# Kernel optimization log

Hardware: AMD Instinct MI355X
Metric: run time of the kernel (lower is better)

## Reference

```python
import jax, jax.numpy as jnp
import numpy as np

BS, T, F, D_IN, NH, D_OUT = 8, 32, 128, 64, 8, 64
GAUSS_STD = 2.0


def setup_inputs() -> dict:
    key = jax.random.key(0)
    ks = jax.random.split(key, 9)
    X = jax.random.normal(ks[0], (BS, F, T, D_IN), dtype=jnp.float32)
    W_query = jax.random.normal(ks[1], (T, F, D_IN, NH, 2), dtype=jnp.float32)
    W_key = jax.random.normal(ks[2], (T, F, D_IN, NH, 2), dtype=jnp.float32)
    Wkey_ = jax.random.normal(ks[3], (T, 2, 2), dtype=jnp.float32)
    u = jax.random.normal(ks[4], (T, F, 2), dtype=jnp.float32)
    attention_center = GAUSS_STD * jax.random.normal(ks[5], (T, NH, 1), dtype=jnp.float32)
    alpha = jax.random.normal(ks[6], (T,), dtype=jnp.float32)
    # relative position features: [F, F, 2] = (delta^2, delta), tiled over T
    rel = (jnp.arange(F)[None, :] - jnp.arange(F)[:, None]).astype(jnp.float32)
    R = jnp.broadcast_to(jnp.stack([rel ** 2, rel], axis=-1)[None], (T, F, F, 2))
    W = jax.random.normal(ks[7], (T, NH * D_IN, D_OUT), dtype=jnp.float32)
    b = jax.random.normal(ks[8], (F, T, D_OUT), dtype=jnp.float32)
    return {"X": X, "W_query": W_query, "W_key": W_key, "Wkey_": Wkey_,
            "u": u, "attention_center": attention_center, "alpha": alpha,
            "R": R, "W": W, "b": b}


def reference(X, W_query, W_key, Wkey_, u, attention_center, alpha, R, W, b):
    # X: [bs, F, T, d_in] -> [bs, T, F, d_in]
    Xp = jnp.transpose(X, (0, 2, 1, 3))
    bs = Xp.shape[0]
    query = jnp.einsum('btfd,tfdhe->btfhe', Xp, W_query)  # [bs,T,F,Nh,2]
    key_t = jnp.einsum('btfd,tfdhe->btfhe', Xp, W_key)    # [bs,T,F,Nh,2]
    r_delta = jnp.einsum('tde,tfle->tfld', Wkey_, R)      # [T,F,F,2]
    centers = jnp.concatenate([jnp.ones_like(attention_center),
                               -2.0 * attention_center], axis=-1)  # [T,Nh,2]
    v = -alpha[:, None, None] * centers                   # [T,Nh,2]
    scores = (jnp.einsum('btfhe,btlhe->btfhl', query, key_t)
              + jnp.einsum('btfhe,tfle->btfhl', query, r_delta)
              + jnp.einsum('tle,btfhe->btfhl', u, key_t)
              + jnp.einsum('the,tfle->tfhl', v, r_delta)[None])  # [bs,T,F,Nh,F]
    probs = jax.nn.softmax(scores, axis=-1)
    vals = jnp.einsum('btfhl,btld->btfhd', probs, Xp)     # [bs,T,F,Nh,d_in]
    vals = vals.reshape(bs, T, F, NH * D_IN)
    out = jnp.einsum('btfd,tdo->bfto', vals, W) + b[None]  # [bs,F,T,d_out]
    return out
```

## Files before the change

kernel.cpp:

```cpp
#include <hip/hip_runtime.h>
#include <hip/hip_bf16.h>

#define NBS 8
#define NT 32
#define NF 128
#define NDIN 64
#define NNH 8
#define NDOUT 64

typedef __bf16 bf16_t;
typedef __bf16 bf16x8 __attribute__((ext_vector_type(8)));
typedef float f32x4 __attribute__((ext_vector_type(4)));

__global__ __launch_bounds__(256, 4)
void qk_project_kernel(const float* __restrict__ X,
                       const float* __restrict__ Wq,
                       const float* __restrict__ Wk,
                       float* __restrict__ q_ws,
                       float* __restrict__ k_ws)
{
    __shared__ float lx[4][8][64];
    const int w = threadIdx.x >> 6, lane = threadIdx.x & 63;
    const int gw = blockIdx.x * 4 + w;
    const int t = gw >> 7, f = gw & 127;

    {
        const int b = lane >> 3, d8 = (lane & 7) << 3;
        const float* src = &X[(((size_t)b * NF + f) * NT + t) * NDIN + d8];
        const float4 v0 = *(const float4*)src;
        const float4 v1 = *(const float4*)(src + 4);
        *(float4*)&lx[w][b][d8]     = v0;
        *(float4*)&lx[w][b][d8 + 4] = v1;
    }
    __syncthreads();

    const int dq = lane >> 4, he = lane & 15;
    const float* wq = Wq + ((size_t)t * NF + f) * (NDIN * 16);
    const float* wk = Wk + ((size_t)t * NF + f) * (NDIN * 16);
    float qa[8] = {0,0,0,0,0,0,0,0}, ka[8] = {0,0,0,0,0,0,0,0};
    for (int d0 = 0; d0 < NDIN; d0 += 4) {
        const int d = d0 + dq;
        const float wqv = wq[d * 16 + he];
        const float wkv = wk[d * 16 + he];
#pragma unroll
        for (int b = 0; b < 8; ++b) {
            const float x = lx[w][b][d];
            qa[b] = fmaf(x, wqv, qa[b]);
            ka[b] = fmaf(x, wkv, ka[b]);
        }
    }
#pragma unroll
    for (int b = 0; b < 8; ++b) {
        qa[b] += __shfl_xor(qa[b], 16); qa[b] += __shfl_xor(qa[b], 32);
        ka[b] += __shfl_xor(ka[b], 16); ka[b] += __shfl_xor(ka[b], 32);
    }
#pragma unroll
    for (int bb = 0; bb < 2; ++bb) {
        const int b = dq + bb * 4;
        q_ws[(((size_t)b * NT + t) * 16 + he) * NF + f] = qa[b];
        k_ws[(((size_t)b * NT + t) * 16 + he) * NF + f] = ka[b];
    }
}

__global__ __launch_bounds__(512, 2)
void spatial_attn_kernel(const float* __restrict__ X,
                         const float* __restrict__ q_ws,
                         const float* __restrict__ k_ws,
                         const float* __restrict__ Wkey,
                         const float* __restrict__ U,
                         const float* __restrict__ AC,
                         const float* __restrict__ Alpha,
                         const float* __restrict__ Wo,
                         const float* __restrict__ Bias,
                         float* __restrict__ Out)
{
    const int blk  = blockIdx.x;
    const int b    = blk & 7;
    const int t    = blk >> 3;
    const int tid  = threadIdx.x;
    const int w    = tid >> 6;
    const int lane = tid & 63;
    const int cq   = lane & 15;
    const int rq   = lane >> 4;
    const int rt   = w;
    const int frow = 16 * rt + cq;

    __shared__ __align__(16) unsigned char smem[142336];
    bf16_t (*XT)[NF + 8]        = (bf16_t (*)[NF + 8])(smem);
    float4 (*kv)[136]           = (float4 (*)[136])(smem + 17408);
    float4 (*qf)[128]           = (float4 (*)[128])(smem + 34816);
    bf16_t (*WTall)[NDOUT][72]  = (bf16_t (*)[NDOUT][72])(smem + 51200);
    bf16_t (*Vscr)[16][68]      = (bf16_t (*)[16][68])(smem + 124928);

#pragma unroll
    for (int r = 0; r < 4; ++r) {
        const int idx = tid + r * 512;
        const int f = idx >> 4, d4 = (idx & 15) << 2;
        const float4 v = *(const float4*)&X[(((size_t)b * NF + f) * NT + t) * NDIN + d4];
        XT[d4 + 0][f] = (bf16_t)v.x; XT[d4 + 1][f] = (bf16_t)v.y;
        XT[d4 + 2][f] = (bf16_t)v.z; XT[d4 + 3][f] = (bf16_t)v.w;
    }
#pragma unroll
    for (int r = 0; r < 2; ++r) {
        const int idx = tid + r * 512;
        const int hh = idx >> 7, l = idx & 127;
        const size_t qkb = ((size_t)b * NT + t) * 16;
        const float k0 = k_ws[(qkb + 2 * hh + 0) * NF + l];
        const float k1 = k_ws[(qkb + 2 * hh + 1) * NF + l];
        const float2 u01 = *(const float2*)&U[((size_t)t * NF + l) * 2];
        kv[hh][17 * (l >> 4) + (l & 15)] = make_float4(k0, k1, u01.x, u01.y);
        const float q0 = q_ws[(qkb + 2 * hh + 0) * NF + l];
        const float q1 = q_ws[(qkb + 2 * hh + 1) * NF + l];
        qf[hh][l] = make_float4(q0, q1, k0, k1);
    }
#pragma unroll
    for (int rep = 0; rep < 16; ++rep) {
        const int flat = rep * 512 + tid;
        const int h = flat >> 10, f10 = flat & 1023;
        const int d = f10 >> 4, o4 = (f10 & 15) << 2;
        const float4 v = *(const float4*)&Wo[((size_t)t * 512 + h * 64 + d) * NDOUT + o4];
        WTall[h][o4 + 0][d] = (bf16_t)v.x; WTall[h][o4 + 1][d] = (bf16_t)v.y;
        WTall[h][o4 + 2][d] = (bf16_t)v.z; WTall[h][o4 + 3][d] = (bf16_t)v.w;
    }

    const float alpha_t = Alpha[t];
    const float wk00 = Wkey[t * 4 + 0], wk01 = Wkey[t * 4 + 1];
    const float wk10 = Wkey[t * 4 + 2], wk11 = Wkey[t * 4 + 3];

    __syncthreads();

    f32x4 oacc[4] = { {0.f,0.f,0.f,0.f}, {0.f,0.f,0.f,0.f}, {0.f,0.f,0.f,0.f}, {0.f,0.f,0.f,0.f} };

#pragma unroll 1
    for (int h = 0; h < NNH; ++h) {
        const float4 qq = qf[h][frow];
        const float q0 = qq.x, q1 = qq.y, kf0 = qq.z, kf1 = qq.w;
        const float v1 = 2.f * alpha_t * AC[t * NNH + h];
        const float c0 = (q0 - alpha_t) * wk00 + (q1 + v1) * wk10;
        const float c1 = (q0 - alpha_t) * wk01 + (q1 + v1) * wk11;

        float sc[4][8];
        float rowmax = -3.0e38f;
#pragma unroll
        for (int kt = 0; kt < 4; ++kt) {
            const int s  = kt * 2 + (rq >> 1);
            const int i0 = (rq & 1) << 3;
            const float4* kvp = &kv[h][17 * s + i0];
            float del = (float)(kt * 32 + rq * 8 - frow);
#pragma unroll
            for (int j = 0; j < 8; ++j) {
                const float4 kj = kvp[j];
                const float sv = q0 * kj.x + q1 * kj.y + kf0 * kj.z + kf1 * kj.w
                               + (c0 * del + c1) * del;
                sc[kt][j] = sv;
                rowmax = fmaxf(rowmax, sv);
                del += 1.f;
            }
        }
        rowmax = fmaxf(rowmax, __shfl_xor(rowmax, 16));
        rowmax = fmaxf(rowmax, __shfl_xor(rowmax, 32));
        float sum = 0.f;
#pragma unroll
        for (int kt = 0; kt < 4; ++kt)
#pragma unroll
            for (int j = 0; j < 8; ++j) {
                sc[kt][j] = __expf(sc[kt][j] - rowmax);
                sum += sc[kt][j];
            }
        sum += __shfl_xor(sum, 16);
        sum += __shfl_xor(sum, 32);
        const float rinv = 1.f / sum;

        f32x4 vacc[4] = { {0.f,0.f,0.f,0.f}, {0.f,0.f,0.f,0.f}, {0.f,0.f,0.f,0.f}, {0.f,0.f,0.f,0.f} };
#pragma unroll
        for (int kt = 0; kt < 4; ++kt) {
            bf16x8 pf;
#pragma unroll
            for (int j = 0; j < 8; ++j) pf[j] = (bf16_t)(sc[kt][j] * rinv);
#pragma unroll
            for (int ct = 0; ct < 4; ++ct) {
                const bf16x8 bb = *(const bf16x8*)&XT[ct * 16 + cq][kt * 32 + rq * 8];
                vacc[ct] = __builtin_amdgcn_mfma_f32_16x16x32_bf16(pf, bb, vacc[ct], 0, 0, 0);
            }
        }
#pragma unroll
        for (int ct = 0; ct < 4; ++ct)
#pragma unroll
            for (int rr = 0; rr < 4; ++rr)
                Vscr[w][rq * 4 + rr][ct * 16 + cq] = (bf16_t)vacc[ct][rr];

#pragma unroll
        for (int kt = 0; kt < 2; ++kt) {
            const bf16x8 a = *(const bf16x8*)&Vscr[w][cq][kt * 32 + rq * 8];
#pragma unroll
            for (int ct = 0; ct < 4; ++ct) {
                const bf16x8 bw = *(const bf16x8*)&WTall[h][ct * 16 + cq][kt * 32 + rq * 8];
                oacc[ct] = __builtin_amdgcn_mfma_f32_16x16x32_bf16(a, bw, oacc[ct], 0, 0, 0);
            }
        }
    }

#pragma unroll
    for (int ct = 0; ct < 4; ++ct) {
#pragma unroll
        for (int rr = 0; rr < 4; ++rr) {
            const int f = 16 * rt + rq * 4 + rr;
            const int o = ct * 16 + cq;
            Out[(((size_t)b * NF + f) * NT + t) * NDOUT + o] =
                oacc[ct][rr] + Bias[((size_t)f * NT + t) * NDOUT + o];
        }
    }
}

extern "C" void kernel_launch(void* const* d_in, const int* in_sizes, int n_in,
                              void* d_out, int out_size, void* d_ws, size_t ws_size,
                              hipStream_t stream) {
    (void)in_sizes; (void)n_in; (void)ws_size; (void)out_size;
    const float* X    = (const float*)d_in[0];
    const float* Wq   = (const float*)d_in[1];
    const float* Wk   = (const float*)d_in[2];
    const float* Wkey = (const float*)d_in[3];
    const float* U    = (const float*)d_in[4];
    const float* AC   = (const float*)d_in[5];
    const float* Al   = (const float*)d_in[6];
    const float* Wo   = (const float*)d_in[8];
    const float* Bias = (const float*)d_in[9];

    float* q_ws = (float*)d_ws;
    float* k_ws = q_ws + (size_t)NBS * NT * 16 * NF;

    qk_project_kernel<<<dim3(NT * NF / 4), dim3(256), 0, stream>>>(X, Wq, Wk, q_ws, k_ws);
    spatial_attn_kernel<<<dim3(NBS * NT), dim3(512), 0, stream>>>(
        X, q_ws, k_ws, Wkey, U, AC, Al, Wo, Bias, (float*)d_out);
}
```

Measured before the change: 54.40 us.

## Split heads across two blocks with atomic output reduction and double-buffered Wo

Each (batch, time) tile is now handled by two blocks that each process four heads, doubling the grid from 256 to 512 blocks. Partial outputs are combined with atomicAdd into an output zeroed by a memset, and only the first head group adds the bias. Wo is streamed per head into a double-buffered, XOR-swizzled shared tile instead of being staged in full, which cuts shared memory enough to allow higher occupancy. The X transpose is swizzled as well. The costs are an extra memset, atomic traffic, a barrier on every head iteration, and X being loaded twice per tile.

```diff
diff --git a/kernel.cpp b/kernel.cpp
--- a/kernel.cpp
+++ b/kernel.cpp
@@ -62,7 +62,7 @@
     }
 }
 
-__global__ __launch_bounds__(512, 2)
+__global__ __launch_bounds__(512, 4)
 void spatial_attn_kernel(const float* __restrict__ X,
                          const float* __restrict__ q_ws,
                          const float* __restrict__ k_ws,
@@ -76,7 +76,9 @@
 {
     const int blk  = blockIdx.x;
     const int b    = blk & 7;
-    const int t    = blk >> 3;
+    const int tq   = blk >> 3;
+    const int hg   = tq & 1;
+    const int t    = tq >> 1;
     const int tid  = threadIdx.x;
     const int w    = tid >> 6;
     const int lane = tid & 63;
@@ -85,42 +87,50 @@
     const int rt   = w;
     const int frow = 16 * rt + cq;
 
-    __shared__ __align__(16) unsigned char smem[142336];
-    bf16_t (*XT)[NF + 8]        = (bf16_t (*)[NF + 8])(smem);
-    float4 (*kv)[136]           = (float4 (*)[136])(smem + 17408);
-    float4 (*qf)[128]           = (float4 (*)[128])(smem + 34816);
-    bf16_t (*WTall)[NDOUT][72]  = (bf16_t (*)[NDOUT][72])(smem + 51200);
-    bf16_t (*Vscr)[16][68]      = (bf16_t (*)[16][68])(smem + 124928);
+    __shared__ __align__(16) unsigned char smem[62992];
+    bf16_t* XTs        = (bf16_t*)smem;
+    float4 (*kv)[136]  = (float4 (*)[136])(smem + 16384);
+    float2 (*qls)[128] = (float2 (*)[128])(smem + 25088);
+    float*  acs        = (float*)(smem + 29184);
+    bf16_t* WTs        = (bf16_t*)(smem + 29200);
+    bf16_t (*Vscr)[16][68] = (bf16_t (*)[16][68])(smem + 45584);
 
 #pragma unroll
     for (int r = 0; r < 4; ++r) {
         const int idx = tid + r * 512;
         const int f = idx >> 4, d4 = (idx & 15) << 2;
         const float4 v = *(const float4*)&X[(((size_t)b * NF + f) * NT + t) * NDIN + d4];
-        XT[d4 + 0][f] = (bf16_t)v.x; XT[d4 + 1][f] = (bf16_t)v.y;
-        XT[d4 + 2][f] = (bf16_t)v.z; XT[d4 + 3][f] = (bf16_t)v.w;
-    }
+        float vv[4]; vv[0] = v.x; vv[1] = v.y; vv[2] = v.z; vv[3] = v.w;
+#pragma unroll
+        for (int i = 0; i < 4; ++i) {
+            const int d = d4 + i;
+            XTs[d * 128 + (((f >> 3) ^ (d & 15)) << 3) + (f & 7)] = (bf16_t)vv[i];
+        }
+    }
+    {
+        const int hh = tid >> 7, l = tid & 127;
+        const int h = hg * 4 + hh;
+        const size_t qkb = ((size_t)b * NT + t) * 16;
+        const float k0 = k_ws[(qkb + 2 * h + 0) * NF + l];
+        const float k1 = k_ws[(qkb + 2 * h + 1) * NF + l];
+        const float2 u01 = *(const float2*)&U[((size_t)t * NF + l) * 2];
+        kv[hh][17 * (l >> 4) + (l & 15)] = make_float4(k0, k1, u01.x, u01.y);
+        const float q0 = q_ws[(qkb + 2 * h + 0) * NF + l];
+        const float q1 = q_ws[(qkb + 2 * h + 1) * NF + l];
+        qls[hh][l] = make_float2(q0, q1);
+    }
+    if (tid < 4) acs[tid] = AC[t * NNH + hg * 4 + tid];
 #pragma unroll
     for (int r = 0; r < 2; ++r) {
         const int idx = tid + r * 512;
-        const int hh = idx >> 7, l = idx & 127;
-        const size_t qkb = ((size_t)b * NT + t) * 16;
-        const float k0 = k_ws[(qkb + 2 * hh + 0) * NF + l];
-        const float k1 = k_ws[(qkb + 2 * hh + 1) * NF + l];
-        const float2 u01 = *(const float2*)&U[((size_t)t * NF + l) * 2];
-        kv[hh][17 * (l >> 4) + (l & 15)] = make_float4(k0, k1, u01.x, u01.y);
-        const float q0 = q_ws[(qkb + 2 * hh + 0) * NF + l];
-        const float q1 = q_ws[(qkb + 2 * hh + 1) * NF + l];
-        qf[hh][l] = make_float4(q0, q1, k0, k1);
-    }
-#pragma unroll
-    for (int rep = 0; rep < 16; ++rep) {
-        const int flat = rep * 512 + tid;
-        const int h = flat >> 10, f10 = flat & 1023;
-        const int d = f10 >> 4, o4 = (f10 & 15) << 2;
-        const float4 v = *(const float4*)&Wo[((size_t)t * 512 + h * 64 + d) * NDOUT + o4];
-        WTall[h][o4 + 0][d] = (bf16_t)v.x; WTall[h][o4 + 1][d] = (bf16_t)v.y;
-        WTall[h][o4 + 2][d] = (bf16_t)v.z; WTall[h][o4 + 3][d] = (bf16_t)v.w;
+        const int dd = idx >> 4, o4 = (idx & 15) << 2;
+        const float4 v = *(const float4*)&Wo[((size_t)t * 512 + (hg * 4) * 64 + dd) * NDOUT + o4];
+        float vv[4]; vv[0] = v.x; vv[1] = v.y; vv[2] = v.z; vv[3] = v.w;
+#pragma unroll
+        for (int i = 0; i < 4; ++i) {
+            const int o = o4 + i;
+            WTs[o * 64 + (((dd >> 3) ^ (o & 7)) << 3) + (dd & 7)] = (bf16_t)vv[i];
+        }
     }
 
     const float alpha_t = Alpha[t];
@@ -132,10 +142,28 @@
     f32x4 oacc[4] = { {0.f,0.f,0.f,0.f}, {0.f,0.f,0.f,0.f}, {0.f,0.f,0.f,0.f}, {0.f,0.f,0.f,0.f} };
 
 #pragma unroll 1
-    for (int h = 0; h < NNH; ++h) {
-        const float4 qq = qf[h][frow];
-        const float q0 = qq.x, q1 = qq.y, kf0 = qq.z, kf1 = qq.w;
-        const float v1 = 2.f * alpha_t * AC[t * NNH + h];
+    for (int th = 0; th < 4; ++th) {
+        if (th < 3) {
+            const int hn = hg * 4 + th + 1;
+            const int bn = ((th + 1) & 1) * 4096;
+#pragma unroll
+            for (int r = 0; r < 2; ++r) {
+                const int idx = tid + r * 512;
+                const int dd = idx >> 4, o4 = (idx & 15) << 2;
+                const float4 v = *(const float4*)&Wo[((size_t)t * 512 + hn * 64 + dd) * NDOUT + o4];
+                float vv[4]; vv[0] = v.x; vv[1] = v.y; vv[2] = v.z; vv[3] = v.w;
+#pragma unroll
+                for (int i = 0; i < 4; ++i) {
+                    const int o = o4 + i;
+                    WTs[bn + o * 64 + (((dd >> 3) ^ (o & 7)) << 3) + (dd & 7)] = (bf16_t)vv[i];
+                }
+            }
+        }
+        const int buf = (th & 1) * 4096;
+        const float2 qq = qls[th][frow];
+        const float4 kk = kv[th][17 * (frow >> 4) + (frow & 15)];
+        const float q0 = qq.x, q1 = qq.y, kf0 = kk.x, kf1 = kk.y;
+        const float v1 = 2.f * alpha_t * acs[th];
         const float c0 = (q0 - alpha_t) * wk00 + (q1 + v1) * wk10;
         const float c1 = (q0 - alpha_t) * wk01 + (q1 + v1) * wk11;
 
@@ -145,7 +173,7 @@
         for (int kt = 0; kt < 4; ++kt) {
             const int s  = kt * 2 + (rq >> 1);
             const int i0 = (rq & 1) << 3;
-            const float4* kvp = &kv[h][17 * s + i0];
+            const float4* kvp = &kv[th][17 * s + i0];
             float del = (float)(kt * 32 + rq * 8 - frow);
 #pragma unroll
             for (int j = 0; j < 8; ++j) {
@@ -179,7 +207,7 @@
             for (int j = 0; j < 8; ++j) pf[j] = (bf16_t)(sc[kt][j] * rinv);
 #pragma unroll
             for (int ct = 0; ct < 4; ++ct) {
-                const bf16x8 bb = *(const bf16x8*)&XT[ct * 16 + cq][kt * 32 + rq * 8];
+                const bf16x8 bb = *(const bf16x8*)&XTs[(ct * 16 + cq) * 128 + (((kt * 4 + rq) ^ cq) << 3)];
                 vacc[ct] = __builtin_amdgcn_mfma_f32_16x16x32_bf16(pf, bb, vacc[ct], 0, 0, 0);
             }
         }
@@ -194,10 +222,11 @@
             const bf16x8 a = *(const bf16x8*)&Vscr[w][cq][kt * 32 + rq * 8];
 #pragma unroll
             for (int ct = 0; ct < 4; ++ct) {
-                const bf16x8 bw = *(const bf16x8*)&WTall[h][ct * 16 + cq][kt * 32 + rq * 8];
+                const bf16x8 bw = *(const bf16x8*)&WTs[buf + (ct * 16 + cq) * 64 + (((kt * 4 + rq) ^ (cq & 7)) << 3)];
                 oacc[ct] = __builtin_amdgcn_mfma_f32_16x16x32_bf16(a, bw, oacc[ct], 0, 0, 0);
             }
         }
+        __syncthreads();
     }
 
 #pragma unroll
@@ -206,8 +235,9 @@
         for (int rr = 0; rr < 4; ++rr) {
             const int f = 16 * rt + rq * 4 + rr;
             const int o = ct * 16 + cq;
-            Out[(((size_t)b * NF + f) * NT + t) * NDOUT + o] =
-                oacc[ct][rr] + Bias[((size_t)f * NT + t) * NDOUT + o];
+            float val = oacc[ct][rr];
+            if (hg == 0) val += Bias[((size_t)f * NT + t) * NDOUT + o];
+            atomicAdd(&Out[(((size_t)b * NF + f) * NT + t) * NDOUT + o], val);
         }
     }
 }
@@ -215,7 +245,7 @@
 extern "C" void kernel_launch(void* const* d_in, const int* in_sizes, int n_in,
                               void* d_out, int out_size, void* d_ws, size_t ws_size,
                               hipStream_t stream) {
-    (void)in_sizes; (void)n_in; (void)ws_size; (void)out_size;
+    (void)in_sizes; (void)n_in; (void)ws_size;
     const float* X    = (const float*)d_in[0];
     const float* Wq   = (const float*)d_in[1];
     const float* Wk   = (const float*)d_in[2];
@@ -229,7 +259,8 @@
     float* q_ws = (float*)d_ws;
     float* k_ws = q_ws + (size_t)NBS * NT * 16 * NF;
 
+    hipMemsetAsync(d_out, 0, (size_t)out_size * sizeof(float), stream);
     qk_project_kernel<<<dim3(NT * NF / 4), dim3(256), 0, stream>>>(X, Wq, Wk, q_ws, k_ws);
-    spatial_attn_kernel<<<dim3(NBS * NT), dim3(512), 0, stream>>>(
+    spatial_attn_kernel<<<dim3(NBS * NT * 2), dim3(512), 0, stream>>>(
         X, q_ws, k_ws, Wkey, U, AC, Al, Wo, Bias, (float*)d_out);
 }
```

New measurement: 132.9 us. 2.44x slower.

## Swizzle shared-memory layouts for XT, WT and key buffers and pack score math

Applied to the files above, without the earlier changes.

Replaces padded shared arrays for the transposed X and W tiles with XOR-swizzled unpadded layouts, and repacks key/u values into pair-interleaved 12-float records so two adjacent score columns load with two float4 reads. Score computation is rewritten on float2 vectors so the compiler can use packed FP32 arithmetic. The aim is fewer LDS bank conflicts, fewer LDS instructions, and fewer scalar FP ops in the softmax stage, at the cost of more complex indexing.

```diff
diff --git a/kernel.cpp b/kernel.cpp
--- a/kernel.cpp
+++ b/kernel.cpp
@@ -11,6 +11,7 @@
 typedef __bf16 bf16_t;
 typedef __bf16 bf16x8 __attribute__((ext_vector_type(8)));
 typedef float f32x4 __attribute__((ext_vector_type(4)));
+typedef float f32x2 __attribute__((ext_vector_type(2)));
 
 __global__ __launch_bounds__(256, 4)
 void qk_project_kernel(const float* __restrict__ X,
@@ -85,20 +86,24 @@
     const int rt   = w;
     const int frow = 16 * rt + cq;
 
-    __shared__ __align__(16) unsigned char smem[142336];
-    bf16_t (*XT)[NF + 8]        = (bf16_t (*)[NF + 8])(smem);
-    float4 (*kv)[136]           = (float4 (*)[136])(smem + 17408);
-    float4 (*qf)[128]           = (float4 (*)[128])(smem + 34816);
-    bf16_t (*WTall)[NDOUT][72]  = (bf16_t (*)[NDOUT][72])(smem + 51200);
-    bf16_t (*Vscr)[16][68]      = (bf16_t (*)[16][68])(smem + 124928);
+    __shared__ __align__(16) unsigned char smem[140288];
+    bf16_t* XTs   = (bf16_t*)smem;
+    float*  kvf   = (float*)(smem + 16384);
+    float4 (*qf)[128] = (float4 (*)[128])(smem + 40960);
+    bf16_t* WTall = (bf16_t*)(smem + 57344);
+    bf16_t (*Vscr)[16][68] = (bf16_t (*)[16][68])(smem + 122880);
 
 #pragma unroll
     for (int r = 0; r < 4; ++r) {
         const int idx = tid + r * 512;
         const int f = idx >> 4, d4 = (idx & 15) << 2;
         const float4 v = *(const float4*)&X[(((size_t)b * NF + f) * NT + t) * NDIN + d4];
-        XT[d4 + 0][f] = (bf16_t)v.x; XT[d4 + 1][f] = (bf16_t)v.y;
-        XT[d4 + 2][f] = (bf16_t)v.z; XT[d4 + 3][f] = (bf16_t)v.w;
+        float vv[4]; vv[0] = v.x; vv[1] = v.y; vv[2] = v.z; vv[3] = v.w;
+#pragma unroll
+        for (int i = 0; i < 4; ++i) {
+            const int d = d4 + i;
+            XTs[d * 128 + (((f >> 3) ^ (d & 15)) << 3) + (f & 7)] = (bf16_t)vv[i];
+        }
     }
 #pragma unroll
     for (int r = 0; r < 2; ++r) {
@@ -107,20 +112,29 @@
         const size_t qkb = ((size_t)b * NT + t) * 16;
         const float k0 = k_ws[(qkb + 2 * hh + 0) * NF + l];
         const float k1 = k_ws[(qkb + 2 * hh + 1) * NF + l];
-        const float2 u01 = *(const float2*)&U[((size_t)t * NF + l) * 2];
-        kv[hh][17 * (l >> 4) + (l & 15)] = make_float4(k0, k1, u01.x, u01.y);
         const float q0 = q_ws[(qkb + 2 * hh + 0) * NF + l];
         const float q1 = q_ws[(qkb + 2 * hh + 1) * NF + l];
+        const float2 u01 = *(const float2*)&U[((size_t)t * NF + l) * 2];
         qf[hh][l] = make_float4(q0, q1, k0, k1);
+        const int P = l >> 1, c = l & 1;
+        const int base = (hh * 64 + P) * 12;
+        kvf[base + 0 + c] = k0;
+        kvf[base + 2 + c] = k1;
+        kvf[base + 4 + c] = u01.x;
+        kvf[base + 6 + c] = u01.y;
     }
 #pragma unroll
     for (int rep = 0; rep < 16; ++rep) {
         const int flat = rep * 512 + tid;
         const int h = flat >> 10, f10 = flat & 1023;
-        const int d = f10 >> 4, o4 = (f10 & 15) << 2;
-        const float4 v = *(const float4*)&Wo[((size_t)t * 512 + h * 64 + d) * NDOUT + o4];
-        WTall[h][o4 + 0][d] = (bf16_t)v.x; WTall[h][o4 + 1][d] = (bf16_t)v.y;
-        WTall[h][o4 + 2][d] = (bf16_t)v.z; WTall[h][o4 + 3][d] = (bf16_t)v.w;
+        const int dd = f10 >> 4, o4 = (f10 & 15) << 2;
+        const float4 v = *(const float4*)&Wo[((size_t)t * 512 + h * 64 + dd) * NDOUT + o4];
+        float vv[4]; vv[0] = v.x; vv[1] = v.y; vv[2] = v.z; vv[3] = v.w;
+#pragma unroll
+        for (int i = 0; i < 4; ++i) {
+            const int o = o4 + i;
+            WTall[h * 4096 + o * 64 + (((dd >> 3) ^ (o & 7)) << 3) + (dd & 7)] = (bf16_t)vv[i];
+        }
     }
 
     const float alpha_t = Alpha[t];
@@ -139,34 +153,41 @@
         const float c0 = (q0 - alpha_t) * wk00 + (q1 + v1) * wk10;
         const float c1 = (q0 - alpha_t) * wk01 + (q1 + v1) * wk11;
 
-        float sc[4][8];
-        float rowmax = -3.0e38f;
+        f32x2 sc2[4][4];
+        f32x2 mx2 = { -3.0e38f, -3.0e38f };
 #pragma unroll
         for (int kt = 0; kt < 4; ++kt) {
-            const int s  = kt * 2 + (rq >> 1);
-            const int i0 = (rq & 1) << 3;
-            const float4* kvp = &kv[h][17 * s + i0];
-            float del = (float)(kt * 32 + rq * 8 - frow);
-#pragma unroll
-            for (int j = 0; j < 8; ++j) {
-                const float4 kj = kvp[j];
-                const float sv = q0 * kj.x + q1 * kj.y + kf0 * kj.z + kf1 * kj.w
-                               + (c0 * del + c1) * del;
-                sc[kt][j] = sv;
-                rowmax = fmaxf(rowmax, sv);
-                del += 1.f;
-            }
-        }
+#pragma unroll
+            for (int j2 = 0; j2 < 4; ++j2) {
+                const int P = kt * 16 + rq * 4 + j2;
+                const float4 ld0 = *(const float4*)&kvf[(h * 64 + P) * 12];
+                const float4 ld1 = *(const float4*)&kvf[(h * 64 + P) * 12 + 4];
+                const f32x2 k0p = { ld0.x, ld0.y };
+                const f32x2 k1p = { ld0.z, ld0.w };
+                const f32x2 u0p = { ld1.x, ld1.y };
+                const f32x2 u1p = { ld1.z, ld1.w };
+                const float l0 = (float)(kt * 32 + rq * 8 + 2 * j2 - frow);
+                const f32x2 delp = { l0, l0 + 1.f };
+                f32x2 sv = k0p * q0 + k1p * q1 + u0p * kf0 + u1p * kf1
+                         + (delp * c0 + c1) * delp;
+                sc2[kt][j2] = sv;
+                mx2 = __builtin_elementwise_max(mx2, sv);
+            }
+        }
+        float rowmax = fmaxf(mx2.x, mx2.y);
         rowmax = fmaxf(rowmax, __shfl_xor(rowmax, 16));
         rowmax = fmaxf(rowmax, __shfl_xor(rowmax, 32));
-        float sum = 0.f;
+        f32x2 s2 = { 0.f, 0.f };
 #pragma unroll
         for (int kt = 0; kt < 4; ++kt)
 #pragma unroll
-            for (int j = 0; j < 8; ++j) {
-                sc[kt][j] = __expf(sc[kt][j] - rowmax);
-                sum += sc[kt][j];
-            }
+            for (int j2 = 0; j2 < 4; ++j2) {
+                f32x2 sv = sc2[kt][j2];
+                const f32x2 e = { __expf(sv.x - rowmax), __expf(sv.y - rowmax) };
+                s2 += e;
+                sc2[kt][j2] = e;
+            }
+        float sum = s2.x + s2.y;
         sum += __shfl_xor(sum, 16);
         sum += __shfl_xor(sum, 32);
         const float rinv = 1.f / sum;
@@ -176,10 +197,14 @@
         for (int kt = 0; kt < 4; ++kt) {
             bf16x8 pf;
 #pragma unroll
-            for (int j = 0; j < 8; ++j) pf[j] = (bf16_t)(sc[kt][j] * rinv);
+            for (int j2 = 0; j2 < 4; ++j2) {
+                const f32x2 e = sc2[kt][j2];
+                pf[2 * j2 + 0] = (bf16_t)(e.x * rinv);
+                pf[2 * j2 + 1] = (bf16_t)(e.y * rinv);
+            }
 #pragma unroll
             for (int ct = 0; ct < 4; ++ct) {
-                const bf16x8 bb = *(const bf16x8*)&XT[ct * 16 + cq][kt * 32 + rq * 8];
+                const bf16x8 bb = *(const bf16x8*)&XTs[(ct * 16 + cq) * 128 + (((kt * 4 + rq) ^ cq) << 3)];
                 vacc[ct] = __builtin_amdgcn_mfma_f32_16x16x32_bf16(pf, bb, vacc[ct], 0, 0, 0);
             }
         }
@@ -194,7 +219,7 @@
             const bf16x8 a = *(const bf16x8*)&Vscr[w][cq][kt * 32 + rq * 8];
 #pragma unroll
             for (int ct = 0; ct < 4; ++ct) {
-                const bf16x8 bw = *(const bf16x8*)&WTall[h][ct * 16 + cq][kt * 32 + rq * 8];
+                const bf16x8 bw = *(const bf16x8*)&WTall[h * 4096 + (ct * 16 + cq) * 64 + (((kt * 4 + rq) ^ (cq & 7)) << 3)];
                 oacc[ct] = __builtin_amdgcn_mfma_f32_16x16x32_bf16(a, bw, oacc[ct], 0, 0, 0);
             }
         }
```

Result: faster. 49.01 us (-9.9%).
